# Optimization experiments

Measured on AMD Instinct MI355X. Metric: run time of the kernel, lower is better.

The kernel has to match this reference:

```python
import jax, jax.numpy as jnp
import numpy as np

H = W = 32
C = 384
NH = 12
HEAD = C // NH
SCALE = HEAD ** -0.5
WS = 8            # window size
SS = 4            # shift size
N = WS * WS       # tokens per window (64)
NW = (H // WS) * (W // WS)  # windows per image (16)
HIDDEN = 4 * C
EPS = 1e-5
SQRT_2_OVER_PI = float(np.sqrt(2.0 / np.pi))


def _relative_position_index():
    ch = np.arange(WS)
    coords = np.stack(np.meshgrid(ch, ch, indexing='ij')).reshape(2, -1)  # [2, N]
    rel = (coords[:, :, None] - coords[:, None, :]).transpose(1, 2, 0)    # [N, N, 2]
    rel[:, :, 0] += WS - 1
    rel[:, :, 1] += WS - 1
    rel[:, :, 0] *= 2 * WS - 1
    return rel.sum(-1)  # [N, N] int


def _attn_mask():
    img = np.zeros((H, W), np.float32)
    sl = (slice(0, -WS), slice(-WS, -SS), slice(-SS, None))
    cnt = 0
    for hs in sl:
        for ws_ in sl:
            img[hs, ws_] = cnt
            cnt += 1
    m = img.reshape(H // WS, WS, W // WS, WS).transpose(0, 2, 1, 3).reshape(-1, N)  # [nW, N]
    am = m[:, None, :] - m[:, :, None]
    return np.where(am != 0, -100.0, 0.0).astype(np.float32)  # [nW, N, N]


REL_IDX = jnp.asarray(_relative_position_index())
ATTN_MASK = jnp.asarray(_attn_mask())


def _gelu(x):
    return x * 0.5 * (1.0 + jnp.tanh(SQRT_2_OVER_PI * (x + 0.044715 * x ** 3)))


def _layernorm(x, g, b):
    mu = jnp.mean(x, axis=-1, keepdims=True)
    var = jnp.mean(jnp.square(x - mu), axis=-1, keepdims=True)
    return (x - mu) * jax.lax.rsqrt(var + EPS) * g + b


def _window_partition(x):  # [B,H,W,C] -> [B*nW, N, C]
    B = x.shape[0]
    x = x.reshape(B, H // WS, WS, W // WS, WS, C).transpose(0, 1, 3, 2, 4, 5)
    return x.reshape(-1, N, C)


def _window_reverse(w, B):  # [B*nW, N, C] -> [B,H,W,C]
    x = w.reshape(B, H // WS, W // WS, WS, WS, C).transpose(0, 1, 3, 2, 4, 5)
    return x.reshape(B, H, W, C)


def setup_inputs() -> dict:
    key = jax.random.key(0)
    ks = jax.random.split(key, 16)
    s = 0.02
    return {
        'x': jax.random.normal(ks[0], (32, H * W, C), jnp.float32),
        'norm1_g': jnp.ones((C,), jnp.float32),
        'norm1_b': jnp.zeros((C,), jnp.float32),
        'qkv_w': jax.random.normal(ks[1], (C, 3 * C), jnp.float32) * s,
        'qkv_b': jnp.zeros((3 * C,), jnp.float32),
        'rel_bias_table': jax.random.normal(ks[2], ((2 * WS - 1) ** 2, NH), jnp.float32) * s,
        'proj_w': jax.random.normal(ks[3], (C, C), jnp.float32) * s,
        'proj_b': jnp.zeros((C,), jnp.float32),
        'norm2_g': jnp.ones((C,), jnp.float32),
        'norm2_b': jnp.zeros((C,), jnp.float32),
        'fc1_w': jax.random.normal(ks[4], (C, HIDDEN), jnp.float32) * s,
        'fc1_b': jnp.zeros((HIDDEN,), jnp.float32),
        'fc2_w': jax.random.normal(ks[5], (HIDDEN, C), jnp.float32) * s,
        'fc2_b': jnp.zeros((C,), jnp.float32),
    }


def reference(x, norm1_g, norm1_b, qkv_w, qkv_b, rel_bias_table, proj_w, proj_b,
              norm2_g, norm2_b, fc1_w, fc1_b, fc2_w, fc2_b):
    B = x.shape[0]
    shortcut = x
    y = _layernorm(x, norm1_g, norm1_b).reshape(B, H, W, C)
    y = jnp.roll(y, shift=(-SS, -SS), axis=(1, 2))          # cyclic shift
    win = _window_partition(y)                               # [B*nW, N, C]

    qkv = (win @ qkv_w + qkv_b).reshape(-1, N, 3, NH, HEAD).transpose(2, 0, 3, 1, 4)
    q, k, v = qkv[0], qkv[1], qkv[2]                         # [B*nW, NH, N, HEAD]
    attn = jnp.einsum('whnd,whmd->whnm', q * SCALE, k)       # [B*nW, NH, N, N]

    bias = rel_bias_table[REL_IDX.reshape(-1)].reshape(N, N, NH).transpose(2, 0, 1)
    attn = attn + bias[None]
    attn = attn.reshape(B, NW, NH, N, N) + ATTN_MASK[None, :, None]
    attn = jax.nn.softmax(attn.reshape(-1, NH, N, N), axis=-1)

    out = jnp.einsum('whnm,whmd->wnhd', attn, v).reshape(-1, N, C)
    out = out @ proj_w + proj_b                              # [B*nW, N, C]

    y = _window_reverse(out, B)
    y = jnp.roll(y, shift=(SS, SS), axis=(1, 2)).reshape(B, H * W, C)

    x = shortcut + y                                         # drop_path is identity (eval)
    h = _layernorm(x, norm2_g, norm2_b)
    h = _gelu(h @ fc1_w + fc1_b) @ fc2_w + fc2_b
    return x + h
```

## Files before the change

### kernel.cpp

```cpp
#include <hip/hip_runtime.h>
#include <hip/hip_bf16.h>
#include <math.h>

typedef __hip_bfloat16 bf16;
typedef __attribute__((ext_vector_type(8))) short short8;
typedef __attribute__((ext_vector_type(4))) float floatx4;

static constexpr int TOK = 32768;
static constexpr int CDIM = 384;
static constexpr int HID = 1536;

__device__ __forceinline__ bf16 f2bf(float v) { return __float2bfloat16(v); }

__device__ __forceinline__ unsigned short bf_bits(float a) {
  bf16 h = __float2bfloat16(a);
  unsigned short u;
  __builtin_memcpy(&u, &h, 2);
  return u;
}
__device__ __forceinline__ unsigned pack2(float a, float b) {
  return (unsigned)bf_bits(a) | ((unsigned)bf_bits(b) << 16);
}

typedef const __attribute__((address_space(1))) unsigned gas_t;
typedef __attribute__((address_space(3))) unsigned las_t;
__device__ __forceinline__ void gload16(const bf16* g, const bf16* l) {
  __builtin_amdgcn_global_load_lds((gas_t*)g, (las_t*)l, 16, 0, 0);
}

__global__ __launch_bounds__(256) void k_convt4(
    const float* __restrict__ s0, bf16* __restrict__ d0,
    const float* __restrict__ s1, bf16* __restrict__ d1,
    const float* __restrict__ s2, bf16* __restrict__ d2,
    const float* __restrict__ s3, bf16* __restrict__ d3) {
  int tid = blockIdx.x * 256 + threadIdx.x;
  const float* src; bf16* dst; int Kd, Nd, off;
  if (tid < 442368) { src = s0; dst = d0; Kd = 384; Nd = 1152; off = tid; }
  else if (tid < 589824) { src = s1; dst = d1; Kd = 384; Nd = 384; off = tid - 442368; }
  else if (tid < 1179648) { src = s2; dst = d2; Kd = 384; Nd = 1536; off = tid - 589824; }
  else { src = s3; dst = d3; Kd = 1536; Nd = 384; off = tid - 1179648; }
  int k = off / Nd, n = off - k * Nd;
  dst[(size_t)n * Kd + k] = f2bf(src[off]);
}

__global__ __launch_bounds__(256) void k_ln1(const float* __restrict__ x,
                                             const float* __restrict__ g,
                                             const float* __restrict__ b,
                                             bf16* __restrict__ out) {
  int wt = blockIdx.x * 4 + (threadIdx.x >> 6);
  int lane = threadIdx.x & 63;
  int win = wt >> 6, ntok = wt & 63;
  int bimg = win >> 4, wi = win & 15;
  int sh = (((wi >> 2) << 3) + (ntok >> 3) + 4) & 31;
  int sw = (((wi & 3) << 3) + (ntok & 7) + 4) & 31;
  const float* xr = x + ((size_t)bimg * 1024 + sh * 32 + sw) * CDIM;
  float v[6]; float s = 0.f, ss = 0.f;
#pragma unroll
  for (int j = 0; j < 6; ++j) {
    float t = xr[j * 64 + lane];
    v[j] = t; s += t; ss += t * t;
  }
#pragma unroll
  for (int off = 32; off > 0; off >>= 1) {
    s += __shfl_xor(s, off, 64);
    ss += __shfl_xor(ss, off, 64);
  }
  float mu = s * (1.f / 384.f);
  float var = ss * (1.f / 384.f) - mu * mu;
  float rs = rsqrtf(var + 1e-5f);
  bf16* orow = out + (size_t)wt * CDIM;
#pragma unroll
  for (int j = 0; j < 6; ++j) {
    int c = j * 64 + lane;
    orow[c] = f2bf((v[j] - mu) * rs * g[c] + b[c]);
  }
}

__global__ __launch_bounds__(256) void k_ln2(const float* __restrict__ x1,
                                             const float* __restrict__ g,
                                             const float* __restrict__ b,
                                             bf16* __restrict__ out) {
  int t = blockIdx.x * 4 + (threadIdx.x >> 6);
  int lane = threadIdx.x & 63;
  const float* xr = x1 + (size_t)t * CDIM;
  float v[6]; float s = 0.f, ss = 0.f;
#pragma unroll
  for (int j = 0; j < 6; ++j) {
    float q = xr[j * 64 + lane];
    v[j] = q; s += q; ss += q * q;
  }
#pragma unroll
  for (int off = 32; off > 0; off >>= 1) {
    s += __shfl_xor(s, off, 64);
    ss += __shfl_xor(ss, off, 64);
  }
  float mu = s * (1.f / 384.f);
  float var = ss * (1.f / 384.f) - mu * mu;
  float rs = rsqrtf(var + 1e-5f);
  bf16* orow = out + (size_t)t * CDIM;
#pragma unroll
  for (int j = 0; j < 6; ++j) {
    int c = j * 64 + lane;
    orow[c] = f2bf((v[j] - mu) * rs * g[c] + b[c]);
  }
}

template <int K, int EPI, int NT>
__global__ __launch_bounds__(256) void k_gemm(const bf16* __restrict__ A,
                                              const bf16* __restrict__ Bt,
                                              const float* __restrict__ bias,
                                              const float* __restrict__ extra,
                                              void* __restrict__ outp) {
  __shared__ __attribute__((aligned(16))) char pool[49152];
  bf16* A0 = (bf16*)pool;
  bf16* B0 = (bf16*)(pool + 8192);
  bf16* A1 = (bf16*)(pool + 16384);
  bf16* B1 = (bf16*)(pool + 24576);
  bf16* A2 = (bf16*)(pool + 32768);
  bf16* B2 = (bf16*)(pool + 40960);

  const int tid = threadIdx.x;
  const int wv = tid >> 6, lane = tid & 63;

  const int flat = blockIdx.x;
  const int xcd = flat & 7;
  const int idx = flat >> 3;
  const int rpx = (gridDim.x >> 3) / NT;
  const int cb = idx % NT;
  const int rb = idx / NT;
  const int mblk = (xcd * rpx + rb) * 128, nblk = cb * 128;

  const int srow = lane >> 3;
  const int sc = (lane & 7) ^ srow;
  const int srow2 = 2 * srow + (sc >> 2);
  const int gco = (sc & 3) * 8;
  const bf16* gaw = A + (size_t)(mblk + wv * 32 + srow2) * K + gco;
  const bf16* gbw = Bt + (size_t)(nblk + wv * 32 + srow2) * K + gco;
  bf16* lA0 = A0 + wv * 1024; bf16* lB0 = B0 + wv * 1024;
  bf16* lA1 = A1 + wv * 1024; bf16* lB1 = B1 + wv * 1024;
  bf16* lA2 = A2 + wv * 1024; bf16* lB2 = B2 + wv * 1024;

  const int wr = wv >> 1, wc = wv & 1;
  const int mr = lane & 15, q = lane >> 4;
  const int slot8 = ((((mr & 1) << 2) | q) ^ (mr >> 1)) * 8;
  const int faOff = (wr * 32 + (mr >> 1)) * 64 + slot8;
  const int fbOff = (wc * 32 + (mr >> 1)) * 64 + slot8;

  floatx4 acc[4][4];
#pragma unroll
  for (int i = 0; i < 4; ++i)
#pragma unroll
    for (int j = 0; j < 4; ++j) acc[i][j] = floatx4{0.f, 0.f, 0.f, 0.f};

#define VM4() asm volatile("s_waitcnt vmcnt(4)" ::: "memory")
#define VM0() asm volatile("s_waitcnt vmcnt(0)" ::: "memory")
#define BAR() __builtin_amdgcn_s_barrier()

#define STAGE(LA, LB, KOFF) do { \
    gload16(gaw + (KOFF), (LA)); \
    gload16(gaw + (KOFF) + 16 * K, (LA) + 512); \
    gload16(gbw + (KOFF), (LB)); \
    gload16(gbw + (KOFF) + 16 * K, (LB) + 512); \
  } while (0)

#define COMPUTE(ABASE, BBASE) do { \
    short8 a_[4], b_[4]; \
    _Pragma("unroll") \
    for (int mt = 0; mt < 4; ++mt) a_[mt] = *(const short8*)((ABASE) + faOff + mt * 512); \
    _Pragma("unroll") \
    for (int nt = 0; nt < 4; ++nt) b_[nt] = *(const short8*)((BBASE) + fbOff + nt * 512); \
    _Pragma("unroll") \
    for (int mt = 0; mt < 4; ++mt) \
      _Pragma("unroll") \
      for (int nt = 0; nt < 4; ++nt) \
        acc[mt][nt] = __builtin_amdgcn_mfma_f32_16x16x32_bf16(a_[mt], b_[nt], acc[mt][nt], 0, 0, 0); \
  } while (0)

  STAGE(lA0, lB0, 0);
  STAGE(lA1, lB1, 32);
  for (int k0 = 0; k0 < K - 96; k0 += 96) {
    VM4(); BAR(); STAGE(lA2, lB2, k0 + 64);  COMPUTE(A0, B0);
    VM4(); BAR(); STAGE(lA0, lB0, k0 + 96);  COMPUTE(A1, B1);
    VM4(); BAR(); STAGE(lA1, lB1, k0 + 128); COMPUTE(A2, B2);
  }
  VM4(); BAR(); STAGE(lA2, lB2, K - 32); COMPUTE(A0, B0);
  VM4(); BAR();                          COMPUTE(A1, B1);
  VM0(); BAR();                          COMPUTE(A2, B2);
#undef STAGE
#undef COMPUTE
#undef VM4
#undef VM0
#undef BAR

  __syncthreads();
  float* epsw = (float*)pool + wv * (16 * 68);
  const int rr = lane >> 2, c0 = (lane & 3) * 16;
#pragma unroll
  for (int mt = 0; mt < 4; ++mt) {
#pragma unroll
    for (int nt = 0; nt < 4; ++nt)
#pragma unroll
      for (int r = 0; r < 4; ++r)
        epsw[(q * 4 + r) * 68 + nt * 16 + mr] = acc[mt][nt][r];
    float v[16];
#pragma unroll
    for (int j = 0; j < 4; ++j) {
      float4 t = *(const float4*)&epsw[rr * 68 + c0 + j * 4];
      v[j * 4 + 0] = t.x; v[j * 4 + 1] = t.y; v[j * 4 + 2] = t.z; v[j * 4 + 3] = t.w;
    }
    const int grow = mblk + wr * 64 + mt * 16 + rr;
    const int gcol = nblk + wc * 64 + c0;

    if constexpr (EPI == 0) {
      int win = grow >> 6, ntok = grow & 63;
      int s = gcol / 384;
      int rem = gcol - s * 384;
      int h = rem >> 5, d0 = rem & 31;
      bf16* op = (bf16*)outp + (((size_t)s * 512 + win) * 12 + h) * 2048 + ntok * 32 + d0;
      uint4 pk;
      float bv[16];
#pragma unroll
      for (int j = 0; j < 16; ++j) bv[j] = v[j] + bias[gcol + j];
      pk.x = pack2(bv[0], bv[1]); pk.y = pack2(bv[2], bv[3]);
      pk.z = pack2(bv[4], bv[5]); pk.w = pack2(bv[6], bv[7]);
      *(uint4*)op = pk;
      pk.x = pack2(bv[8], bv[9]); pk.y = pack2(bv[10], bv[11]);
      pk.z = pack2(bv[12], bv[13]); pk.w = pack2(bv[14], bv[15]);
      *(uint4*)(op + 8) = pk;
    } else if constexpr (EPI == 1) {
      int win = grow >> 6, ntok = grow & 63;
      int bimg = win >> 4, wi = win & 15;
      int hh = (((wi >> 2) << 3) + (ntok >> 3) + 4) & 31;
      int ww = (((wi & 3) << 3) + (ntok & 7) + 4) & 31;
      size_t t = (size_t)bimg * 1024 + hh * 32 + ww;
      float* op = (float*)outp + t * CDIM + gcol;
      const float* xr = extra + t * CDIM + gcol;
#pragma unroll
      for (int j = 0; j < 4; ++j) {
        float4 xv = *(const float4*)(xr + j * 4);
        float4 ov;
        ov.x = xv.x + v[j * 4 + 0] + bias[gcol + j * 4 + 0];
        ov.y = xv.y + v[j * 4 + 1] + bias[gcol + j * 4 + 1];
        ov.z = xv.z + v[j * 4 + 2] + bias[gcol + j * 4 + 2];
        ov.w = xv.w + v[j * 4 + 3] + bias[gcol + j * 4 + 3];
        *(float4*)(op + j * 4) = ov;
      }
    }
  }
}

__global__ __launch_bounds__(512, 2) void k_mlp(const bf16* __restrict__ A,
                                                const bf16* __restrict__ W1t,
                                                const bf16* __restrict__ W2t,
                                                const float* __restrict__ b1,
                                                const float* __restrict__ b2,
                                                const float* __restrict__ x1,
                                                float* __restrict__ out) {
  __shared__ __attribute__((aligned(16))) char pool[131072];
  bf16* A0 = (bf16*)pool;
  bf16* A1 = (bf16*)(pool + 8192);
  bf16* A2 = (bf16*)(pool + 16384);
  bf16* W10 = (bf16*)(pool + 24576);
  bf16* W11 = (bf16*)(pool + 32768);
  bf16* W12 = (bf16*)(pool + 40960);
  bf16* hs = (bf16*)(pool + 49152);
  bf16* W2sA = (bf16*)(pool + 81920);
  bf16* W2sB = (bf16*)(pool + 106496);

  const int tid = threadIdx.x;
  const int wv = tid >> 6, lane = tid & 63;
  const int mblk = blockIdx.x * 128;

  const int srow = lane >> 3;
  const int sc = (lane & 7) ^ srow;
  const int srow2 = 2 * srow + (sc >> 2);
  const int gco = (sc & 3) * 8;

  const bf16* ga = A + (size_t)(mblk + wv * 16 + srow2) * 384 + gco;
  const bf16* g1 = W1t + (size_t)(wv * 16 + srow2) * 384 + gco;
  const bf16* g2 = W2t + (size_t)(wv * 48 + srow2) * 1536 + gco;

  const int wr1 = wv >> 2, wc1 = wv & 3;
  const int mr = lane & 15, q = lane >> 4;
  const int slot8 = ((((mr & 1) << 2) | q) ^ (mr >> 1)) * 8;
  const int faOff1 = (wr1 * 32 + (mr >> 1)) * 64 + slot8;
  const int fbOff1 = (wc1 * 16 + (mr >> 1)) * 64 + slot8;
  const int fbOff2 = (wc1 * 48 + (mr >> 1)) * 64 + slot8;
  const size_t hb = (size_t)(wr1 * 64 + mr) * 128;
  int px[4];
#pragma unroll
  for (int kk = 0; kk < 4; ++kk)
    px[kk] = (((kk & 2) << 2) | ((((kk & 1) << 2) | q) ^ (mr & 7))) * 8;

  floatx4 acc1[4][2];
  floatx4 acc2[4][6];
#pragma unroll
  for (int i = 0; i < 4; ++i) {
#pragma unroll
    for (int j = 0; j < 2; ++j) acc1[i][j] = floatx4{0.f, 0.f, 0.f, 0.f};
#pragma unroll
    for (int j = 0; j < 6; ++j) acc2[i][j] = floatx4{0.f, 0.f, 0.f, 0.f};
  }

#define VMW(N) asm volatile("s_waitcnt vmcnt(" #N ")" ::: "memory")
#define LGKM0() asm volatile("s_waitcnt lgkmcnt(0)" ::: "memory")
#define BARR() __builtin_amdgcn_s_barrier()
#define ST(ABUF, WBUF, G1P, KO) do { \
    gload16(ga + (KO), (ABUF) + wv * 512); \
    gload16((G1P) + (KO), (WBUF) + wv * 512); \
  } while (0)
#define STW2(BUF, KK, G2P) do { \
    _Pragma("unroll") \
    for (int g = 0; g < 3; ++g) \
      gload16((G2P) + (KK) * 32 + (size_t)g * 16 * 1536, (BUF) + wv * 1536 + g * 512); \
  } while (0)
#define C1(AB, WB) do { \
    short8 a_[4], b_[2]; \
    _Pragma("unroll") \
    for (int mt = 0; mt < 4; ++mt) a_[mt] = *(const short8*)((AB) + faOff1 + mt * 512); \
    b_[0] = *(const short8*)((WB) + fbOff1); \
    b_[1] = *(const short8*)((WB) + fbOff1 + 512); \
    _Pragma("unroll") \
    for (int mt = 0; mt < 4; ++mt) \
      _Pragma("unroll") \
      for (int nt = 0; nt < 2; ++nt) \
        acc1[mt][nt] = __builtin_amdgcn_mfma_f32_16x16x32_bf16(a_[mt], b_[nt], acc1[mt][nt], 0, 0, 0); \
  } while (0)
#define C2(BUF, KK) do { \
    short8 ha[4], wb[6]; \
    _Pragma("unroll") \
    for (int mt = 0; mt < 4; ++mt) \
      ha[mt] = *(const short8*)(hs + hb + mt * 2048 + px[KK]); \
    _Pragma("unroll") \
    for (int nt = 0; nt < 6; ++nt) \
      wb[nt] = *(const short8*)((BUF) + fbOff2 + nt * 512); \
    _Pragma("unroll") \
    for (int mt = 0; mt < 4; ++mt) \
      _Pragma("unroll") \
      for (int nt = 0; nt < 6; ++nt) \
        acc2[mt][nt] = __builtin_amdgcn_mfma_f32_16x16x32_bf16(ha[mt], wb[nt], acc2[mt][nt], 0, 0, 0); \
  } while (0)
#define GELU_H(BB0, BB1) do { \
    _Pragma("unroll") \
    for (int mt = 0; mt < 4; ++mt) { \
      const int tokb = wr1 * 64 + mt * 16 + q * 4; \
      _Pragma("unroll") \
      for (int nt = 0; nt < 2; ++nt) { \
        const float bb = nt ? (BB1) : (BB0); \
        const int sw = wc1 * 4 + nt * 2 + (mr >> 3); \
        const int s8 = sw & 8, s7 = sw & 7; \
        _Pragma("unroll") \
        for (int r = 0; r < 4; ++r) { \
          float z = acc1[mt][nt][r] + bb; \
          float t2 = z * z; \
          float cp = __builtin_fmaf(t2, -0.0713548162f, -1.5957691216f); \
          float e = __expf(z * cp); \
          float gl = z * __builtin_amdgcn_rcpf(1.f + e); \
          const int t7 = ((q & 1) << 2) | r; \
          hs[(size_t)(tokb + r) * 128 + (s8 | (s7 ^ t7)) * 8 + (mr & 7)] = f2bf(gl); \
        } \
        acc1[mt][nt] = floatx4{0.f, 0.f, 0.f, 0.f}; \
      } \
    } \
    LGKM0(); \
  } while (0)

  {
    float bb0 = b1[wc1 * 32 + mr];
    float bb1 = b1[wc1 * 32 + 16 + mr];
    ST(A0, W10, g1, 0);
    ST(A1, W11, g1, 32);
    const bf16* g1n = g1 + 49152;
    VMW(2); BARR(); ST(A2, W12, g1, 64);                       C1(A0, W10);
    VMW(2); BARR(); ST(A0, W10, g1, 96);                       C1(A1, W11);
    VMW(2); BARR(); ST(A1, W11, g1, 128);                      C1(A2, W12);
    VMW(2); BARR(); ST(A2, W12, g1, 160);                      C1(A0, W10);
    VMW(2); BARR(); ST(A0, W10, g1, 192);                      C1(A1, W11);
    VMW(2); BARR(); ST(A1, W11, g1, 224);                      C1(A2, W12);
    VMW(2); BARR(); ST(A2, W12, g1, 256); STW2(W2sA, 0, g2);   C1(A0, W10);
    VMW(5); BARR(); ST(A0, W10, g1, 288);                      C1(A1, W11);
    VMW(5); BARR(); ST(A1, W11, g1, 320); STW2(W2sB, 1, g2);   C1(A2, W12);
    VMW(5); BARR(); ST(A2, W12, g1, 352);                      C1(A0, W10);
    VMW(5); BARR(); ST(A0, W10, g1n, 0);                       C1(A1, W11);
    VMW(2); BARR(); ST(A1, W11, g1n, 32);                      C1(A2, W12);
    GELU_H(bb0, bb1);
    g1 += 49152;
  }

  for (int ci = 1; ci < 12; ++ci) {
    float bb0 = b1[ci * 128 + wc1 * 32 + mr];
    float bb1 = b1[ci * 128 + wc1 * 32 + 16 + mr];
    const bf16* g1n = g1 + 49152;
    const bf16* g2n = g2 + 128;
    VMW(4); BARR(); ST(A2, W12, g1, 64);                        C1(A0, W10);
    VMW(4); BARR(); ST(A0, W10, g1, 96);                        C1(A1, W11); C2(W2sA, 0);
    VMW(2); BARR(); ST(A1, W11, g1, 128); STW2(W2sA, 2, g2);    C1(A2, W12);
    VMW(5); BARR(); ST(A2, W12, g1, 160);                       C1(A0, W10); C2(W2sB, 1);
    VMW(5); BARR(); ST(A0, W10, g1, 192); STW2(W2sB, 3, g2);    C1(A1, W11);
    VMW(5); BARR(); ST(A1, W11, g1, 224);                       C1(A2, W12); C2(W2sA, 2);
    VMW(5); BARR(); ST(A2, W12, g1, 256); STW2(W2sA, 0, g2n);   C1(A0, W10);
    VMW(5); BARR(); ST(A0, W10, g1, 288);                       C1(A1, W11); C2(W2sB, 3);
    VMW(5); BARR(); ST(A1, W11, g1, 320); STW2(W2sB, 1, g2n);   C1(A2, W12);
    VMW(5); BARR(); ST(A2, W12, g1, 352);                       C1(A0, W10);
    VMW(5); BARR(); ST(A0, W10, g1n, 0);                        C1(A1, W11);
    VMW(2); BARR(); ST(A1, W11, g1n, 32);                       C1(A2, W12);
    GELU_H(bb0, bb1);
    g1 += 49152;
    g2 += 128;
  }

  VMW(0); BARR();
  C2(W2sA, 0);
  BARR();
  STW2(W2sA, 2, g2);
  C2(W2sB, 1);
  BARR();
  STW2(W2sB, 3, g2);
  VMW(3); BARR();
  C2(W2sA, 2);
  VMW(0); BARR();
  C2(W2sB, 3);
#undef ST
#undef STW2
#undef C1
#undef C2
#undef GELU_H

  __syncthreads();

  float* epsw = (float*)(pool + wv * 6400);
  const int rr = lane >> 2, c4 = (lane & 3) * 24;
#pragma unroll
  for (int mt = 0; mt < 4; ++mt) {
#pragma unroll
    for (int nt = 0; nt < 6; ++nt)
#pragma unroll
      for (int r = 0; r < 4; ++r)
        epsw[(q * 4 + r) * 100 + nt * 16 + mr] = acc2[mt][nt][r];
    const int grow = mblk + wr1 * 64 + mt * 16 + rr;
    const int gcol = wc1 * 96 + c4;
    const float* xr = x1 + (size_t)grow * 384 + gcol;
    float* op = out + (size_t)grow * 384 + gcol;
#pragma unroll
    for (int j = 0; j < 6; ++j) {
      float4 t = *(const float4*)&epsw[rr * 100 + c4 + j * 4];
      float4 xv = *(const float4*)(xr + j * 4);
      float4 bv = *(const float4*)&b2[gcol + j * 4];
      float4 ov;
      ov.x = xv.x + t.x + bv.x;
      ov.y = xv.y + t.y + bv.y;
      ov.z = xv.z + t.z + bv.z;
      ov.w = xv.w + t.w + bv.w;
      *(float4*)(op + j * 4) = ov;
    }
  }
#undef VMW
#undef LGKM0
#undef BARR
}

__global__ __launch_bounds__(64) void k_attn(const bf16* __restrict__ qkv,
                                             const float* __restrict__ tblg,
                                             bf16* __restrict__ out) {
  __shared__ __attribute__((aligned(16))) char pool[16384];
  bf16* Qs = (bf16*)pool;
  bf16* Ks = (bf16*)(pool + 5120);
  bf16* Ps = (bf16*)pool;
  float* Os = (float*)pool;
  bf16* Vt = (bf16*)(pool + 10240);
  unsigned long long* msk = (unsigned long long*)(pool + 14848);
  float* tbl = (float*)(pool + 15360);

  const int bid = blockIdx.x;
  const int win = bid / 12, head = bid - win * 12;
  const int lane = threadIdx.x;
  const int q = lane >> 4, mr = lane & 15;

  for (int i = lane; i < 225; i += 64) tbl[i] = tblg[i * 12 + head];

  size_t base = ((size_t)win * 12 + head) * 2048 + lane * 32;
  const uint4* qp = (const uint4*)(qkv + base);
  const uint4* kp = (const uint4*)(qkv + (size_t)12582912 + base);
  const uint4* vp = (const uint4*)(qkv + (size_t)25165824 + base);
#pragma unroll
  for (int i = 0; i < 4; ++i) *(uint4*)(Qs + lane * 40 + i * 8) = qp[i];
#pragma unroll
  for (int i = 0; i < 4; ++i) *(uint4*)(Ks + lane * 40 + i * 8) = kp[i];
  {
    union { uint4 u[4]; unsigned short h[32]; } vv;
#pragma unroll
    for (int i = 0; i < 4; ++i) vv.u[i] = vp[i];
    unsigned short* VtU = (unsigned short*)Vt;
#pragma unroll
    for (int d = 0; d < 32; ++d) VtU[d * 72 + lane] = vv.h[d];
  }
  {
    int wi = win & 15;
    int ri = lane >> 3, ci = lane & 7;
    int rh = ((wi >> 2) << 3) + ri, rw = ((wi & 3) << 3) + ci;
    int rid = (rh < 24 ? 0 : (rh < 28 ? 1 : 2)) * 3 + (rw < 24 ? 0 : (rw < 28 ? 1 : 2));
    unsigned long long m = 0;
#pragma unroll
    for (int v = 0; v < 9; ++v) {
      unsigned long long bb = __ballot(rid == v);
      if (rid == v) m = bb;
    }
    msk[lane] = m;
  }

  floatx4 sac[4][4];
#pragma unroll
  for (int i = 0; i < 4; ++i)
#pragma unroll
    for (int j = 0; j < 4; ++j) sac[i][j] = floatx4{0.f, 0.f, 0.f, 0.f};
  {
    short8 af[4], bf[4];
#pragma unroll
    for (int t = 0; t < 4; ++t) af[t] = *(const short8*)(Qs + (t * 16 + mr) * 40 + q * 8);
#pragma unroll
    for (int t = 0; t < 4; ++t) bf[t] = *(const short8*)(Ks + (t * 16 + mr) * 40 + q * 8);
#pragma unroll
    for (int mt = 0; mt < 4; ++mt)
#pragma unroll
      for (int nt = 0; nt < 4; ++nt)
        sac[mt][nt] = __builtin_amdgcn_mfma_f32_16x16x32_bf16(af[mt], bf[nt], sac[mt][nt], 0, 0, 0);
  }

  float psum[4][4];
#pragma unroll
  for (int mt = 0; mt < 4; ++mt)
#pragma unroll
    for (int r = 0; r < 4; ++r) psum[mt][r] = 0.f;
#pragma unroll
  for (int mt = 0; mt < 4; ++mt) {
#pragma unroll
    for (int r = 0; r < 4; ++r) {
      const int i = mt * 16 + q * 4 + r;
      const unsigned long long mrow = msk[i];
      const int bi = (i >> 3) * 15 + (i & 7);
#pragma unroll
      for (int nt = 0; nt < 4; ++nt) {
        const int j = nt * 16 + mr;
        const int idx = bi + 112 - (j >> 3) * 15 - (j & 7);
        float val = sac[mt][nt][r] * 0.17677669529663687f + tbl[idx];
        float p = __expf(val);
        p = ((mrow >> j) & 1ull) ? p : 0.f;
        psum[mt][r] += p;
        Ps[i * 72 + j] = f2bf(p);
      }
    }
  }
  float inv[4][4];
#pragma unroll
  for (int mt = 0; mt < 4; ++mt)
#pragma unroll
    for (int r = 0; r < 4; ++r) {
      float s = psum[mt][r];
      s += __shfl_xor(s, 1, 64);
      s += __shfl_xor(s, 2, 64);
      s += __shfl_xor(s, 4, 64);
      s += __shfl_xor(s, 8, 64);
      inv[mt][r] = 1.f / s;
    }

  floatx4 oac[4][2];
#pragma unroll
  for (int i = 0; i < 4; ++i)
#pragma unroll
    for (int j = 0; j < 2; ++j) oac[i][j] = floatx4{0.f, 0.f, 0.f, 0.f};
#pragma unroll
  for (int kk = 0; kk < 2; ++kk) {
    short8 ap[4], bv[2];
#pragma unroll
    for (int mt = 0; mt < 4; ++mt)
      ap[mt] = *(const short8*)(Ps + (mt * 16 + mr) * 72 + kk * 32 + q * 8);
#pragma unroll
    for (int nt = 0; nt < 2; ++nt)
      bv[nt] = *(const short8*)(Vt + (nt * 16 + mr) * 72 + kk * 32 + q * 8);
#pragma unroll
    for (int mt = 0; mt < 4; ++mt)
#pragma unroll
      for (int nt = 0; nt < 2; ++nt)
        oac[mt][nt] = __builtin_amdgcn_mfma_f32_16x16x32_bf16(ap[mt], bv[nt], oac[mt][nt], 0, 0, 0);
  }

#pragma unroll
  for (int mt = 0; mt < 4; ++mt)
#pragma unroll
    for (int nt = 0; nt < 2; ++nt)
#pragma unroll
      for (int r = 0; r < 4; ++r)
        Os[(mt * 16 + q * 4 + r) * 40 + nt * 16 + mr] = oac[mt][nt][r] * inv[mt][r];
  float ov[32];
#pragma unroll
  for (int c = 0; c < 8; ++c) {
    const int cc = c ^ (lane & 7);
    float4 t = *(const float4*)(Os + lane * 40 + cc * 4);
    ov[cc * 4 + 0] = t.x; ov[cc * 4 + 1] = t.y;
    ov[cc * 4 + 2] = t.z; ov[cc * 4 + 3] = t.w;
  }
  uint4* o4 = (uint4*)(out + ((size_t)win * 64 + lane) * CDIM + head * 32);
#pragma unroll
  for (int i = 0; i < 4; ++i) {
    uint4 pk;
    pk.x = pack2(ov[i * 8 + 0], ov[i * 8 + 1]);
    pk.y = pack2(ov[i * 8 + 2], ov[i * 8 + 3]);
    pk.z = pack2(ov[i * 8 + 4], ov[i * 8 + 5]);
    pk.w = pack2(ov[i * 8 + 6], ov[i * 8 + 7]);
    o4[i] = pk;
  }
}

extern "C" void kernel_launch(void* const* d_in, const int* in_sizes, int n_in,
                              void* d_out, int out_size, void* d_ws, size_t ws_size,
                              hipStream_t stream) {
  const float* x = (const float*)d_in[0];
  const float* n1g = (const float*)d_in[1];
  const float* n1b = (const float*)d_in[2];
  const float* qkv_w = (const float*)d_in[3];
  const float* qkv_b = (const float*)d_in[4];
  const float* reltbl = (const float*)d_in[5];
  const float* proj_w = (const float*)d_in[6];
  const float* proj_b = (const float*)d_in[7];
  const float* n2g = (const float*)d_in[8];
  const float* n2b = (const float*)d_in[9];
  const float* fc1_w = (const float*)d_in[10];
  const float* fc1_b = (const float*)d_in[11];
  const float* fc2_w = (const float*)d_in[12];
  const float* fc2_b = (const float*)d_in[13];
  float* out = (float*)d_out;

  char* p = (char*)d_ws;
  bf16* w_qkv_t = (bf16*)p;  p += (size_t)442368 * 2;
  bf16* w_proj_t = (bf16*)p; p += (size_t)147456 * 2;
  bf16* w_fc1_t = (bf16*)p;  p += (size_t)589824 * 2;
  bf16* w_fc2_t = (bf16*)p;  p += (size_t)589824 * 2;
  bf16* bufA = (bf16*)p;     p += (size_t)12582912 * 2;
  bf16* qkvb = (bf16*)p;     p += (size_t)37748736 * 2;
  bf16* attno = (bf16*)p;    p += (size_t)12582912 * 2;
  float* x1 = (float*)p;     p += (size_t)12582912 * 4;

  k_convt4<<<dim3(6912), dim3(256), 0, stream>>>(qkv_w, w_qkv_t, proj_w, w_proj_t,
                                                 fc1_w, w_fc1_t, fc2_w, w_fc2_t);

  k_ln1<<<dim3(8192), dim3(256), 0, stream>>>(x, n1g, n1b, bufA);
  k_gemm<384, 0, 9><<<dim3(9 * 256), dim3(256), 0, stream>>>(bufA, w_qkv_t, qkv_b, nullptr, qkvb);
  k_attn<<<dim3(6144), dim3(64), 0, stream>>>(qkvb, reltbl, attno);
  k_gemm<384, 1, 3><<<dim3(3 * 256), dim3(256), 0, stream>>>(attno, w_proj_t, proj_b, x, x1);
  k_ln2<<<dim3(8192), dim3(256), 0, stream>>>(x1, n2g, n2b, bufA);
  k_mlp<<<dim3(256), dim3(512), 0, stream>>>(bufA, w_fc1_t, w_fc2_t, fc1_b, fc2_b, x1, out);
}
```

Measured before the change: 396.8 us.

## Serialize fc2 chunk after fc1 in MLP loop and raise MFMA priority in attention

The fused MLP kernel previously interleaved the second GEMM (fc2) chunk loads and MFMAs with the next fc1 chunk's pipeline. It now runs each hidden chunk's fc1 pipeline, GELU and full sync, then the fc2 chunk, which simplifies the wait counts and lowers register and LDS contention. This gives up the overlap between the two GEMMs and adds a block-wide barrier per chunk. Separately, the attention kernel wraps its MFMA blocks in s_setprio to favour matrix issue across waves.

```diff
diff --git a/kernel.cpp b/kernel.cpp
--- a/kernel.cpp
+++ b/kernel.cpp
@@ -365,67 +365,55 @@
     LGKM0(); \
   } while (0)
 
-  {
-    float bb0 = b1[wc1 * 32 + mr];
-    float bb1 = b1[wc1 * 32 + 16 + mr];
-    ST(A0, W10, g1, 0);
-    ST(A1, W11, g1, 32);
+  ST(A0, W10, g1, 0);
+  ST(A1, W11, g1, 32);
+
+  for (int ci = 0; ci < 12; ++ci) {
+    BARR();
+    const int cb = ci * 128;
+    float bb0 = b1[cb + wc1 * 32 + mr];
+    float bb1 = b1[cb + wc1 * 32 + 16 + mr];
+    STW2(W2sA, 0, g2);
+    STW2(W2sB, 1, g2);
+
     const bf16* g1n = g1 + 49152;
-    VMW(2); BARR(); ST(A2, W12, g1, 64);                       C1(A0, W10);
-    VMW(2); BARR(); ST(A0, W10, g1, 96);                       C1(A1, W11);
-    VMW(2); BARR(); ST(A1, W11, g1, 128);                      C1(A2, W12);
-    VMW(2); BARR(); ST(A2, W12, g1, 160);                      C1(A0, W10);
-    VMW(2); BARR(); ST(A0, W10, g1, 192);                      C1(A1, W11);
-    VMW(2); BARR(); ST(A1, W11, g1, 224);                      C1(A2, W12);
-    VMW(2); BARR(); ST(A2, W12, g1, 256); STW2(W2sA, 0, g2);   C1(A0, W10);
-    VMW(5); BARR(); ST(A0, W10, g1, 288);                      C1(A1, W11);
-    VMW(5); BARR(); ST(A1, W11, g1, 320); STW2(W2sB, 1, g2);   C1(A2, W12);
-    VMW(5); BARR(); ST(A2, W12, g1, 352);                      C1(A0, W10);
-    VMW(5); BARR(); ST(A0, W10, g1n, 0);                       C1(A1, W11);
-    VMW(2); BARR(); ST(A1, W11, g1n, 32);                      C1(A2, W12);
+    VMW(8); BARR(); ST(A2, W12, g1, 64);   C1(A0, W10);
+    VMW(8); BARR(); ST(A0, W10, g1, 96);   C1(A1, W11);
+    VMW(2); BARR(); ST(A1, W11, g1, 128);  C1(A2, W12);
+    VMW(2); BARR(); ST(A2, W12, g1, 160);  C1(A0, W10);
+    VMW(2); BARR(); ST(A0, W10, g1, 192);  C1(A1, W11);
+    VMW(2); BARR(); ST(A1, W11, g1, 224);  C1(A2, W12);
+    VMW(2); BARR(); ST(A2, W12, g1, 256);  C1(A0, W10);
+    VMW(2); BARR(); ST(A0, W10, g1, 288);  C1(A1, W11);
+    VMW(2); BARR(); ST(A1, W11, g1, 320);  C1(A2, W12);
+    VMW(2); BARR(); ST(A2, W12, g1, 352);  C1(A0, W10);
+    VMW(2); BARR(); ST(A0, W10, g1n, 0);   C1(A1, W11);
+    VMW(2); BARR(); ST(A1, W11, g1n, 32);  C1(A2, W12);
+
     GELU_H(bb0, bb1);
-    g1 += 49152;
-  }
-
-  for (int ci = 1; ci < 12; ++ci) {
-    float bb0 = b1[ci * 128 + wc1 * 32 + mr];
-    float bb1 = b1[ci * 128 + wc1 * 32 + 16 + mr];
-    const bf16* g1n = g1 + 49152;
-    const bf16* g2n = g2 + 128;
-    VMW(4); BARR(); ST(A2, W12, g1, 64);                        C1(A0, W10);
-    VMW(4); BARR(); ST(A0, W10, g1, 96);                        C1(A1, W11); C2(W2sA, 0);
-    VMW(2); BARR(); ST(A1, W11, g1, 128); STW2(W2sA, 2, g2);    C1(A2, W12);
-    VMW(5); BARR(); ST(A2, W12, g1, 160);                       C1(A0, W10); C2(W2sB, 1);
-    VMW(5); BARR(); ST(A0, W10, g1, 192); STW2(W2sB, 3, g2);    C1(A1, W11);
-    VMW(5); BARR(); ST(A1, W11, g1, 224);                       C1(A2, W12); C2(W2sA, 2);
-    VMW(5); BARR(); ST(A2, W12, g1, 256); STW2(W2sA, 0, g2n);   C1(A0, W10);
-    VMW(5); BARR(); ST(A0, W10, g1, 288);                       C1(A1, W11); C2(W2sB, 3);
-    VMW(5); BARR(); ST(A1, W11, g1, 320); STW2(W2sB, 1, g2n);   C1(A2, W12);
-    VMW(5); BARR(); ST(A2, W12, g1, 352);                       C1(A0, W10);
-    VMW(5); BARR(); ST(A0, W10, g1n, 0);                        C1(A1, W11);
-    VMW(2); BARR(); ST(A1, W11, g1n, 32);                       C1(A2, W12);
-    GELU_H(bb0, bb1);
+    __syncthreads();
+
+    C2(W2sA, 0);
+    BARR();
+    STW2(W2sA, 2, g2);
+    C2(W2sB, 1);
+    BARR();
+    STW2(W2sB, 3, g2);
+    VMW(3); BARR();
+    C2(W2sA, 2);
+    VMW(0); BARR();
+    C2(W2sB, 3);
+
     g1 += 49152;
     g2 += 128;
   }
-
-  VMW(0); BARR();
-  C2(W2sA, 0);
-  BARR();
-  STW2(W2sA, 2, g2);
-  C2(W2sB, 1);
-  BARR();
-  STW2(W2sB, 3, g2);
-  VMW(3); BARR();
-  C2(W2sA, 2);
-  VMW(0); BARR();
-  C2(W2sB, 3);
 #undef ST
 #undef STW2
 #undef C1
 #undef C2
 #undef GELU_H
 
+  VMW(0);
   __syncthreads();
 
   float* epsw = (float*)(pool + wv * 6400);
@@ -519,11 +507,13 @@
     for (int t = 0; t < 4; ++t) af[t] = *(const short8*)(Qs + (t * 16 + mr) * 40 + q * 8);
 #pragma unroll
     for (int t = 0; t < 4; ++t) bf[t] = *(const short8*)(Ks + (t * 16 + mr) * 40 + q * 8);
+    __builtin_amdgcn_s_setprio(1);
 #pragma unroll
     for (int mt = 0; mt < 4; ++mt)
 #pragma unroll
       for (int nt = 0; nt < 4; ++nt)
         sac[mt][nt] = __builtin_amdgcn_mfma_f32_16x16x32_bf16(af[mt], bf[nt], sac[mt][nt], 0, 0, 0);
+    __builtin_amdgcn_s_setprio(0);
   }
 
   float psum[4][4];
@@ -577,11 +567,13 @@
 #pragma unroll
     for (int nt = 0; nt < 2; ++nt)
       bv[nt] = *(const short8*)(Vt + (nt * 16 + mr) * 72 + kk * 32 + q * 8);
+    __builtin_amdgcn_s_setprio(1);
 #pragma unroll
     for (int mt = 0; mt < 4; ++mt)
 #pragma unroll
       for (int nt = 0; nt < 2; ++nt)
         oac[mt][nt] = __builtin_amdgcn_mfma_f32_16x16x32_bf16(ap[mt], bv[nt], oac[mt][nt], 0, 0, 0);
+    __builtin_amdgcn_s_setprio(0);
   }
 
 #pragma unroll
```

Result: no change. 392.0 us (-1.2%).
